# Kernel optimization log

Hardware: AMD Instinct MI355X
Metric: run time of the kernel (lower is better)

Reference implementation:

```python
import jax, jax.numpy as jnp
import numpy as np

SIGMA = 25.0
B = 4096            # number of graphs
N = 1048576         # total nodes across batch
FEAT = 44           # node feature dim
TED = 84            # t_embed_dim = 128 - 44


def setup_inputs() -> dict:
    key = jax.random.key(0)
    ks = jax.random.split(key, 12)
    # ragged graph sizes via sorted random cut points -> ptr of length B+1
    cuts = jnp.sort(jax.random.randint(ks[0], (B - 1,), 0, N))
    ptr = jnp.concatenate([jnp.zeros((1,), jnp.int32), cuts.astype(jnp.int32), jnp.full((1,), N, jnp.int32)])
    node_attr = jax.random.normal(ks[1], (N, FEAT), dtype=jnp.float32)
    t = jax.random.uniform(ks[2], (B,), dtype=jnp.float32, minval=1e-3, maxval=1.0)
    # GaussianFourierProjection buffer (requires_grad=False in torch)
    W_f = jax.random.normal(ks[3], (TED // 2,), dtype=jnp.float32) * 30.0
    # embed Linear 84->84
    embed_w = jax.random.normal(ks[4], (TED, TED), dtype=jnp.float32) / np.sqrt(TED)
    embed_b = jax.random.normal(ks[5], (TED,), dtype=jnp.float32) * 0.01
    # Linear chain 128->64->32->4 (torch convention: W [out, in])
    w0 = jax.random.normal(ks[6], (64, 128), dtype=jnp.float32) / np.sqrt(128)
    b0 = jax.random.normal(ks[7], (64,), dtype=jnp.float32) * 0.01
    w1 = jax.random.normal(ks[8], (32, 64), dtype=jnp.float32) / np.sqrt(64)
    b1 = jax.random.normal(ks[9], (32,), dtype=jnp.float32) * 0.01
    w2 = jax.random.normal(ks[10], (4, 32), dtype=jnp.float32) / np.sqrt(32)
    b2 = jax.random.normal(ks[11], (4,), dtype=jnp.float32) * 0.01
    return {"node_attr": node_attr, "t": t, "ptr": ptr, "W_f": W_f,
            "embed_w": embed_w, "embed_b": embed_b,
            "w0": w0, "b0": b0, "w1": w1, "b1": b1, "w2": w2, "b2": b2}


def reference(node_attr, t, ptr, W_f, embed_w, embed_b, w0, b0, w1, b1, w2, b2):
    swish = lambda x: x * jax.nn.sigmoid(x)
    # GaussianFourierProjection: [B, TED]
    x_proj = t[:, None] * W_f[None, :] * (2.0 * np.pi)
    t_emb = jnp.concatenate([jnp.sin(x_proj), jnp.cos(x_proj)], axis=-1)
    embed = swish(t_emb @ embed_w.T + embed_b)                      # [B, TED]
    # ragged broadcast: graph id per node (replaces the torch per-graph tile loop)
    seg = jnp.searchsorted(ptr, jnp.arange(node_attr.shape[0], dtype=ptr.dtype), side='right') - 1
    h = jnp.concatenate([node_attr, embed[seg]], axis=-1)           # [N, 128]
    h = swish(h @ w0.T + b0)                                        # [N, 64]
    h = swish(h @ w1.T + b1)                                        # [N, 32]
    h = swish(h @ w2.T + b2)                                        # [N, 4]
    std = jnp.sqrt((SIGMA ** (2.0 * t) - 1.0) / (2.0 * np.log(SIGMA)))  # [B]
    return h / std[seg][:, None]
```

## Files before the change

kernel.cpp:

```cpp
#include <hip/hip_runtime.h>
#include <hip/hip_fp16.h>

typedef _Float16 f16x8 __attribute__((ext_vector_type(8)));
typedef __fp16   fp16x2 __attribute__((ext_vector_type(2)));
typedef float f32x4 __attribute__((ext_vector_type(4)));

#define FEAT 44
#define TED  84
#define MT   128
#define WN   32
#define NBLK 768
#define BUFB 6144

__global__ void seg_prep(const int* __restrict__ gptr, int* __restrict__ seg) {
    int g = blockIdx.x;
    int a = gptr[g], b = gptr[g + 1];
    for (int i = a + threadIdx.x; i < b; i += 256) seg[i] = g;
}

__global__ void embed_prep(const float* __restrict__ t_arr, const float* __restrict__ W_f,
                           const float* __restrict__ embed_w, const float* __restrict__ embed_b,
                           const float* __restrict__ w0, const float* __restrict__ b0,
                           const float* __restrict__ w1, const float* __restrict__ w2,
                           float* __restrict__ emb0, float* __restrict__ inv_std,
                           _Float16* __restrict__ w0h, _Float16* __restrict__ w1h,
                           _Float16* __restrict__ w2h, int B) {
    int g   = blockIdx.x;
    int tid = threadIdx.x;
    if (g == B) {
        for (int i = tid; i < 64 * 64; i += 128) {
            int o = i >> 6, k = i & 63;
            w0h[i] = (k < FEAT) ? (_Float16)w0[o * 128 + k] : (_Float16)0.f;
        }
        for (int i = tid; i < 32 * 64; i += 128) w1h[i] = (_Float16)w1[i];
        for (int i = tid; i < 16 * 32; i += 128) w2h[i] = (i < 4 * 32) ? (_Float16)w2[i] : (_Float16)0.f;
        return;
    }
    __shared__ float temb[TED];
    __shared__ float ses[TED];
    float tv = t_arr[g];
    if (tid < TED) {
        int j   = (tid < TED / 2) ? tid : tid - TED / 2;
        float x = tv * W_f[j] * 6.283185307179586f;
        temb[tid] = (tid < TED / 2) ? sinf(x) : cosf(x);
    }
    __syncthreads();
    if (tid < TED) {
        const float* wr = embed_w + tid * TED;
        float s = embed_b[tid];
        #pragma unroll 4
        for (int j = 0; j < TED; ++j) s = fmaf(temb[j], wr[j], s);
        ses[tid] = s / (1.0f + __expf(-s));
    }
    if (tid == TED) {
        const float c = 6.437751649736401f;
        inv_std[g] = rsqrtf(expm1f(c * tv) / c);
    }
    __syncthreads();
    if (tid < 64) {
        const float* wr = w0 + tid * 128 + FEAT;
        float s = b0[tid];
        #pragma unroll 4
        for (int j = 0; j < TED; ++j) s = fmaf(ses[j], wr[j], s);
        emb0[g * 64 + tid] = s;
    }
}

__device__ __forceinline__ float swishf(float x) {
    float e = __builtin_amdgcn_exp2f(x * -1.4426950408889634f);
    return x * __builtin_amdgcn_rcpf(1.0f + e);
}

__device__ __forceinline__ int ubound(const int* __restrict__ p, int n, int v) {
    int lo = 0, hi = n;
    while (lo < hi) { int m = (lo + hi) >> 1; if (p[m] <= v) lo = m + 1; else hi = m; }
    return lo - 1;
}

__device__ __forceinline__ void stage_attr(const float* __restrict__ node_attr, int row0,
                                           const char* lim, char* dst, int lane) {
    const char* g = (const char*)node_attr + (size_t)row0 * (FEAT * 4);
    #pragma unroll
    for (int k = 0; k < 6; ++k) {
        const char* s = g + k * 1024 + lane * 16;
        if (s > lim) s = lim;
        __builtin_amdgcn_global_load_lds(
            (const __attribute__((address_space(1))) unsigned int*)s,
            (__attribute__((address_space(3))) unsigned int*)(dst + k * 1024),
            16, 0, 0);
    }
}

template<bool USE_SEG>
__global__ __launch_bounds__(256)
void scorenet_main(const float* __restrict__ node_attr,
                   const int* __restrict__ gptr, int B,
                   const int* __restrict__ seg_arr,
                   const float* __restrict__ emb0,
                   const float* __restrict__ inv_std_g,
                   const _Float16* __restrict__ w0h,
                   const _Float16* __restrict__ w1h,
                   const _Float16* __restrict__ w2h,
                   const float* __restrict__ b1,
                   const float* __restrict__ b2,
                   float* __restrict__ out, int ntiles, int nbytes_attr) {
    __shared__ __align__(16) char lds[2 * BUFB * 4];

    const int t    = threadIdx.x;
    const int lane = t & 63;
    const int wid  = t >> 6;
    const int lr   = lane & 15;
    const int lk   = lane >> 4;
    const char* lim = (const char*)node_attr + nbytes_attr - 16;

    char* buf_cur = lds + wid * (2 * BUFB);
    char* buf_nxt = buf_cur + BUFB;

    int tile = blockIdx.x;
    if (tile >= ntiles) return;
    const int stride = gridDim.x;

    f16x8 aw0[2][4];
    #pragma unroll
    for (int kt = 0; kt < 2; ++kt)
        #pragma unroll
        for (int mt = 0; mt < 4; ++mt)
            aw0[kt][mt] = *(const f16x8*)(w0h + (mt * 16 + lr) * 64 + kt * 32 + lk * 8);
    f16x8 aw1[2][2];
    #pragma unroll
    for (int kt = 0; kt < 2; ++kt)
        #pragma unroll
        for (int mt = 0; mt < 2; ++mt)
            aw1[kt][mt] = *(const f16x8*)(w1h + (mt * 16 + lr) * 64 + kt * 32 + lk * 8);
    f16x8 aw2 = *(const f16x8*)(w2h + lr * 32 + lk * 8);
    f32x4 bias1f[2];
    #pragma unroll
    for (int mt = 0; mt < 2; ++mt) {
        float4 bv = *(const float4*)(b1 + mt * 16 + lk * 4);
        bias1f[mt] = f32x4{bv.x, bv.y, bv.z, bv.w};
    }
    float4 b2vv = *(const float4*)b2;
    const f32x4 c2init = (lk == 0) ? f32x4{b2vv.x, b2vv.y, b2vv.z, b2vv.w} : f32x4{0.f, 0.f, 0.f, 0.f};

    stage_attr(node_attr, tile * MT + wid * WN, lim, buf_cur, lane);
    int seg0, seg1;
    {
        int wb = tile * MT + wid * WN;
        if (USE_SEG) { seg0 = seg_arr[wb + lr]; seg1 = seg_arr[wb + 16 + lr]; }
        else { seg0 = ubound(gptr, B + 1, wb + lr); seg1 = ubound(gptr, B + 1, wb + 16 + lr); }
    }

    while (tile < ntiles) {
        const int wb   = tile * MT + wid * WN;
        int tpf = tile + stride; if (tpf >= ntiles) tpf = tile;
        const int nwb  = tpf * MT + wid * WN;

        float is0 = inv_std_g[seg0];
        float is1 = inv_std_g[seg1];
        f32x4 acc0[4][2];
        #pragma unroll
        for (int mt = 0; mt < 4; ++mt) {
            acc0[mt][0] = *(const f32x4*)(emb0 + seg0 * 64 + mt * 16 + lk * 4);
            acc0[mt][1] = *(const f32x4*)(emb0 + seg1 * 64 + mt * 16 + lk * 4);
        }

        stage_attr(node_attr, nwb, lim, buf_nxt, lane);

        int ns0, ns1;
        if (USE_SEG) { ns0 = seg_arr[nwb + lr]; ns1 = seg_arr[nwb + 16 + lr]; }
        else { ns0 = ubound(gptr, B + 1, nwb + lr); ns1 = ubound(gptr, B + 1, nwb + 16 + lr); }

        asm volatile("s_waitcnt vmcnt(18)" ::: "memory");
        __builtin_amdgcn_sched_barrier(0);

        union u8 { fp16x2 h2[4]; f16x8 v; };
        f16x8 bf[2][2];
        #pragma unroll
        for (int nt = 0; nt < 2; ++nt) {
            const float4* rowp = (const float4*)(buf_cur + (nt * 16 + lr) * (FEAT * 4));
            float4 a = rowp[lk * 2];
            float4 b = rowp[lk * 2 + 1];
            float4 c = make_float4(0.f, 0.f, 0.f, 0.f);
            float4 d = make_float4(0.f, 0.f, 0.f, 0.f);
            if (lk == 0) { c = rowp[8]; d = rowp[9]; }
            else if (lk == 1) { c = rowp[10]; }
            u8 f0, f1;
            f0.h2[0] = __builtin_amdgcn_cvt_pkrtz(a.x, a.y);
            f0.h2[1] = __builtin_amdgcn_cvt_pkrtz(a.z, a.w);
            f0.h2[2] = __builtin_amdgcn_cvt_pkrtz(b.x, b.y);
            f0.h2[3] = __builtin_amdgcn_cvt_pkrtz(b.z, b.w);
            f1.h2[0] = __builtin_amdgcn_cvt_pkrtz(c.x, c.y);
            f1.h2[1] = __builtin_amdgcn_cvt_pkrtz(c.z, c.w);
            f1.h2[2] = __builtin_amdgcn_cvt_pkrtz(d.x, d.y);
            f1.h2[3] = __builtin_amdgcn_cvt_pkrtz(d.z, d.w);
            bf[nt][0] = f0.v;
            bf[nt][1] = f1.v;
        }

        #pragma unroll
        for (int kt = 0; kt < 2; ++kt)
            #pragma unroll
            for (int mt = 0; mt < 4; ++mt)
                #pragma unroll
                for (int nt = 0; nt < 2; ++nt)
                    acc0[mt][nt] = __builtin_amdgcn_mfma_f32_16x16x32_f16(aw0[kt][mt], bf[nt][kt], acc0[mt][nt], 0, 0, 0);

        #pragma unroll
        for (int mt = 0; mt < 4; ++mt)
            #pragma unroll
            for (int nt = 0; nt < 2; ++nt) {
                int j = nt * 16 + lr;
                union { fp16x2 h2[2]; uint2 u; } p;
                p.h2[0] = __builtin_amdgcn_cvt_pkrtz(swishf(acc0[mt][nt][0]), swishf(acc0[mt][nt][1]));
                p.h2[1] = __builtin_amdgcn_cvt_pkrtz(swishf(acc0[mt][nt][2]), swishf(acc0[mt][nt][3]));
                int addr = j * 128 + (mt * 16 + lk * 4) * 2;
                *(uint2*)(buf_cur + (addr ^ ((j & 7) << 4))) = p.u;
            }

        f32x4 acc1[2][2];
        #pragma unroll
        for (int mt = 0; mt < 2; ++mt) { acc1[mt][0] = bias1f[mt]; acc1[mt][1] = bias1f[mt]; }
        #pragma unroll
        for (int kt = 0; kt < 2; ++kt) {
            f16x8 bx[2];
            #pragma unroll
            for (int nt = 0; nt < 2; ++nt) {
                int j    = nt * 16 + lr;
                int addr = j * 128 + kt * 64 + lk * 16;
                bx[nt] = *(const f16x8*)(buf_cur + (addr ^ ((j & 7) << 4)));
            }
            #pragma unroll
            for (int mt = 0; mt < 2; ++mt)
                #pragma unroll
                for (int nt = 0; nt < 2; ++nt)
                    acc1[mt][nt] = __builtin_amdgcn_mfma_f32_16x16x32_f16(aw1[kt][mt], bx[nt], acc1[mt][nt], 0, 0, 0);
        }

        #pragma unroll
        for (int mt = 0; mt < 2; ++mt)
            #pragma unroll
            for (int nt = 0; nt < 2; ++nt) {
                int j = nt * 16 + lr;
                union { fp16x2 h2[2]; uint2 u; } p;
                p.h2[0] = __builtin_amdgcn_cvt_pkrtz(swishf(acc1[mt][nt][0]), swishf(acc1[mt][nt][1]));
                p.h2[1] = __builtin_amdgcn_cvt_pkrtz(swishf(acc1[mt][nt][2]), swishf(acc1[mt][nt][3]));
                int addr = 4096 + j * 64 + (mt * 16 + lk * 4) * 2;
                *(uint2*)(buf_cur + (addr ^ ((j & 3) << 4))) = p.u;
            }

        f32x4 acc2[2] = {c2init, c2init};
        #pragma unroll
        for (int nt = 0; nt < 2; ++nt) {
            int j    = nt * 16 + lr;
            int addr = 4096 + j * 64 + lk * 16;
            f16x8 bx = *(const f16x8*)(buf_cur + (addr ^ ((j & 3) << 4)));
            acc2[nt] = __builtin_amdgcn_mfma_f32_16x16x32_f16(aw2, bx, acc2[nt], 0, 0, 0);
        }
        if (lk == 0) {
            #pragma unroll
            for (int nt = 0; nt < 2; ++nt) {
                int j = nt * 16 + lr;
                float is = nt ? is1 : is0;
                float4 o;
                o.x = swishf(acc2[nt][0]) * is;
                o.y = swishf(acc2[nt][1]) * is;
                o.z = swishf(acc2[nt][2]) * is;
                o.w = swishf(acc2[nt][3]) * is;
                *(float4*)(out + (size_t)(wb + j) * 4) = o;
            }
        }

        { char* tmp = buf_cur; buf_cur = buf_nxt; buf_nxt = tmp; }
        seg0 = ns0; seg1 = ns1;
        tile += stride;
    }
}

extern "C" void kernel_launch(void* const* d_in, const int* in_sizes, int n_in,
                              void* d_out, int out_size, void* d_ws, size_t ws_size,
                              hipStream_t stream) {
    const float* node_attr = (const float*)d_in[0];
    const float* t_arr     = (const float*)d_in[1];
    const int*   gptr      = (const int*)d_in[2];
    const float* W_f       = (const float*)d_in[3];
    const float* embed_w   = (const float*)d_in[4];
    const float* embed_b   = (const float*)d_in[5];
    const float* w0        = (const float*)d_in[6];
    const float* b0        = (const float*)d_in[7];
    const float* w1        = (const float*)d_in[8];
    const float* b1        = (const float*)d_in[9];
    const float* w2        = (const float*)d_in[10];
    const float* b2        = (const float*)d_in[11];
    float* out = (float*)d_out;

    const int N = in_sizes[0] / FEAT;
    const int B = in_sizes[2] - 1;
    const int ntiles = N / MT;
    const int nbytes_attr = in_sizes[0] * 4;

    char* ws = (char*)d_ws;
    size_t off = 0;
    float*    emb0    = (float*)(ws + off); off += (size_t)B * 64 * sizeof(float);
    off = (off + 1023) & ~(size_t)1023;
    float*    inv_std = (float*)(ws + off); off += (size_t)B * sizeof(float);
    off = (off + 1023) & ~(size_t)1023;
    _Float16* w0h = (_Float16*)(ws + off);  off += 64 * 64 * sizeof(_Float16);
    _Float16* w1h = (_Float16*)(ws + off);  off += 32 * 64 * sizeof(_Float16);
    _Float16* w2h = (_Float16*)(ws + off);  off += 16 * 32 * sizeof(_Float16);
    off = (off + 1023) & ~(size_t)1023;
    int* seg = (int*)(ws + off);
    size_t need_with_seg = off + (size_t)N * sizeof(int);
    bool use_seg = (ws_size >= need_with_seg);

    const int grid = (ntiles < NBLK) ? ntiles : NBLK;

    embed_prep<<<B + 1, 128, 0, stream>>>(t_arr, W_f, embed_w, embed_b, w0, b0, w1, w2,
                                          emb0, inv_std, w0h, w1h, w2h, B);
    if (use_seg) {
        seg_prep<<<B, 256, 0, stream>>>(gptr, seg);
        scorenet_main<true><<<grid, 256, 0, stream>>>(node_attr, gptr, B, seg, emb0, inv_std,
                                                      w0h, w1h, w2h, b1, b2, out, ntiles, nbytes_attr);
    } else {
        scorenet_main<false><<<grid, 256, 0, stream>>>(node_attr, gptr, B, seg, emb0, inv_std,
                                                       w0h, w1h, w2h, b1, b2, out, ntiles, nbytes_attr);
    }
}
```

Before: 87.15 us.

## Fuse segment-id prep into embed prep kernel and prefetch segment ids two tiles ahead

Measured after the change: 83.83 us. -3.8%, faster.

```diff
diff --git a/kernel.cpp b/kernel.cpp
--- a/kernel.cpp
+++ b/kernel.cpp
@@ -12,19 +12,14 @@
 #define NBLK 768
 #define BUFB 6144
 
-__global__ void seg_prep(const int* __restrict__ gptr, int* __restrict__ seg) {
-    int g = blockIdx.x;
-    int a = gptr[g], b = gptr[g + 1];
-    for (int i = a + threadIdx.x; i < b; i += 256) seg[i] = g;
-}
-
-__global__ void embed_prep(const float* __restrict__ t_arr, const float* __restrict__ W_f,
-                           const float* __restrict__ embed_w, const float* __restrict__ embed_b,
-                           const float* __restrict__ w0, const float* __restrict__ b0,
-                           const float* __restrict__ w1, const float* __restrict__ w2,
-                           float* __restrict__ emb0, float* __restrict__ inv_std,
-                           _Float16* __restrict__ w0h, _Float16* __restrict__ w1h,
-                           _Float16* __restrict__ w2h, int B) {
+__global__ void prep_all(const float* __restrict__ t_arr, const float* __restrict__ W_f,
+                         const float* __restrict__ embed_w, const float* __restrict__ embed_b,
+                         const float* __restrict__ w0, const float* __restrict__ b0,
+                         const float* __restrict__ w1, const float* __restrict__ w2,
+                         const int* __restrict__ gptr, int* __restrict__ seg, int do_seg,
+                         float* __restrict__ emb0, float* __restrict__ inv_std,
+                         _Float16* __restrict__ w0h, _Float16* __restrict__ w1h,
+                         _Float16* __restrict__ w2h, int B) {
     int g   = blockIdx.x;
     int tid = threadIdx.x;
     if (g == B) {
@@ -35,6 +30,10 @@
         for (int i = tid; i < 32 * 64; i += 128) w1h[i] = (_Float16)w1[i];
         for (int i = tid; i < 16 * 32; i += 128) w2h[i] = (i < 4 * 32) ? (_Float16)w2[i] : (_Float16)0.f;
         return;
+    }
+    if (do_seg) {
+        int a = gptr[g], b = gptr[g + 1];
+        for (int i = a + tid; i < b; i += 128) seg[i] = g;
     }
     __shared__ float temb[TED];
     __shared__ float ses[TED];
@@ -113,11 +112,7 @@
     const int lk   = lane >> 4;
     const char* lim = (const char*)node_attr + nbytes_attr - 16;
 
-    char* buf_cur = lds + wid * (2 * BUFB);
-    char* buf_nxt = buf_cur + BUFB;
-
-    int tile = blockIdx.x;
-    if (tile >= ntiles) return;
+    if (blockIdx.x >= ntiles) return;
     const int stride = gridDim.x;
 
     f16x8 aw0[2][4];
@@ -142,35 +137,47 @@
     float4 b2vv = *(const float4*)b2;
     const f32x4 c2init = (lk == 0) ? f32x4{b2vv.x, b2vv.y, b2vv.z, b2vv.w} : f32x4{0.f, 0.f, 0.f, 0.f};
 
+    char* buf_cur = lds + wid * (2 * BUFB);
+    char* buf_nxt = buf_cur + BUFB;
+
+    int tile = blockIdx.x;
+
     stage_attr(node_attr, tile * MT + wid * WN, lim, buf_cur, lane);
-    int seg0, seg1;
+    int s0, s1, n0, n1;
     {
         int wb = tile * MT + wid * WN;
-        if (USE_SEG) { seg0 = seg_arr[wb + lr]; seg1 = seg_arr[wb + 16 + lr]; }
-        else { seg0 = ubound(gptr, B + 1, wb + lr); seg1 = ubound(gptr, B + 1, wb + 16 + lr); }
+        if (USE_SEG) { s0 = seg_arr[wb + lr]; s1 = seg_arr[wb + 16 + lr]; }
+        else { s0 = ubound(gptr, B + 1, wb + lr); s1 = ubound(gptr, B + 1, wb + 16 + lr); }
+        int t1 = tile + stride; if (t1 >= ntiles) t1 = tile;
+        int wb1 = t1 * MT + wid * WN;
+        if (USE_SEG) { n0 = seg_arr[wb1 + lr]; n1 = seg_arr[wb1 + 16 + lr]; }
+        else { n0 = ubound(gptr, B + 1, wb1 + lr); n1 = ubound(gptr, B + 1, wb1 + 16 + lr); }
     }
 
     while (tile < ntiles) {
-        const int wb   = tile * MT + wid * WN;
-        int tpf = tile + stride; if (tpf >= ntiles) tpf = tile;
-        const int nwb  = tpf * MT + wid * WN;
-
-        float is0 = inv_std_g[seg0];
-        float is1 = inv_std_g[seg1];
+        const int wb = tile * MT + wid * WN;
+        int tp1 = tile + stride;     if (tp1 >= ntiles) tp1 = tile;
+        int tp2 = tile + 2 * stride; if (tp2 >= ntiles) tp2 = tile;
+
+        float is0 = inv_std_g[s0];
+        float is1 = inv_std_g[s1];
         f32x4 acc0[4][2];
         #pragma unroll
         for (int mt = 0; mt < 4; ++mt) {
-            acc0[mt][0] = *(const f32x4*)(emb0 + seg0 * 64 + mt * 16 + lk * 4);
-            acc0[mt][1] = *(const f32x4*)(emb0 + seg1 * 64 + mt * 16 + lk * 4);
-        }
-
-        stage_attr(node_attr, nwb, lim, buf_nxt, lane);
-
-        int ns0, ns1;
-        if (USE_SEG) { ns0 = seg_arr[nwb + lr]; ns1 = seg_arr[nwb + 16 + lr]; }
-        else { ns0 = ubound(gptr, B + 1, nwb + lr); ns1 = ubound(gptr, B + 1, nwb + 16 + lr); }
-
-        asm volatile("s_waitcnt vmcnt(18)" ::: "memory");
+            acc0[mt][0] = *(const f32x4*)(emb0 + s0 * 64 + mt * 16 + lk * 4);
+            acc0[mt][1] = *(const f32x4*)(emb0 + s1 * 64 + mt * 16 + lk * 4);
+        }
+
+        stage_attr(node_attr, tp1 * MT + wid * WN, lim, buf_nxt, lane);
+
+        int m0, m1;
+        {
+            int wb2 = tp2 * MT + wid * WN;
+            if (USE_SEG) { m0 = seg_arr[wb2 + lr]; m1 = seg_arr[wb2 + 16 + lr]; }
+            else { m0 = ubound(gptr, B + 1, wb2 + lr); m1 = ubound(gptr, B + 1, wb2 + 16 + lr); }
+        }
+
+        asm volatile("s_waitcnt vmcnt(20)" ::: "memory");
         __builtin_amdgcn_sched_barrier(0);
 
         union u8 { fp16x2 h2[4]; f16x8 v; };
@@ -271,7 +278,7 @@
         }
 
         { char* tmp = buf_cur; buf_cur = buf_nxt; buf_nxt = tmp; }
-        seg0 = ns0; seg1 = ns1;
+        s0 = n0; s1 = n1; n0 = m0; n1 = m1;
         tile += stride;
     }
 }
@@ -314,10 +321,10 @@
 
     const int grid = (ntiles < NBLK) ? ntiles : NBLK;
 
-    embed_prep<<<B + 1, 128, 0, stream>>>(t_arr, W_f, embed_w, embed_b, w0, b0, w1, w2,
-                                          emb0, inv_std, w0h, w1h, w2h, B);
+    prep_all<<<B + 1, 128, 0, stream>>>(t_arr, W_f, embed_w, embed_b, w0, b0, w1, w2,
+                                        gptr, seg, use_seg ? 1 : 0,
+                                        emb0, inv_std, w0h, w1h, w2h, B);
     if (use_seg) {
-        seg_prep<<<B, 256, 0, stream>>>(gptr, seg);
         scorenet_main<true><<<grid, 256, 0, stream>>>(node_attr, gptr, B, seg, emb0, inv_std,
                                                       w0h, w1h, w2h, b1, b2, out, ntiles, nbytes_attr);
     } else {
```
